# Kernel optimization log

Hardware: AMD Instinct MI355X
Metric: run time of the kernel (lower is better)

The kernel has to match this reference:

```python
import jax, jax.numpy as jnp
import numpy as np

B, S, D = 256, 512, 128
NQ, NC, NQD, NCD = 20000, 2000, 101, 101


def setup_inputs() -> dict:
    key = jax.random.key(0)
    ks = jax.random.split(key, 32)
    s = 0.05
    inp = {
        "question_seq": jax.random.randint(ks[0], (B, S), 0, NQ),
        "concept_seq": jax.random.randint(ks[1], (B, S), 0, NC),
        "question_diff_seq": jax.random.randint(ks[2], (B, S), 0, NQD),
        "concept_diff_seq": jax.random.randint(ks[3], (B, S), 0, NCD),
        "correct_seq": jax.random.randint(ks[4], (B, S), 0, 2),
        "E_q": jax.random.normal(ks[5], (NQ, D)) * s,
        "E_c": jax.random.normal(ks[6], (NC, D)) * s,
        "E_qd": jax.random.normal(ks[7], (NQD, D)) * s,
        "E_cd": jax.random.normal(ks[8], (NCD, D)) * s,
        "E_corr": jax.random.normal(ks[9], (2, D)) * s,
        "Wx": jax.random.normal(ks[10], (4 * D, D)) * s,
        "bx": jnp.zeros((D,)),
        "W_s1": jax.random.normal(ks[11], (D, D)) * s,
        "b_s1": jnp.zeros((D,)),
        "W_s2": jax.random.normal(ks[12], (D, D)) * s,
        "b_s2": jnp.zeros((D,)),
        "W_p1": jax.random.normal(ks[13], (2 * D, D)) * s,
        "b_p1": jnp.zeros((D,)),
        "W_p2": jax.random.normal(ks[14], (2 * D, D)) * s,
        "b_p2": jnp.zeros((D,)),
        "W_ki": jax.random.normal(ks[15], (4 * D, D)) * s,
        "b_ki": jnp.zeros((D,)),
        # xavier_uniform init of h_pre: bound = sqrt(6/(fan_in+fan_out))
        "h0": jax.random.uniform(ks[16], (B, D), minval=-1.0, maxval=1.0) * np.sqrt(6.0 / (B + D)),
    }
    return inp


def reference(question_seq, concept_seq, question_diff_seq, concept_diff_seq,
              correct_seq, E_q, E_c, E_qd, E_cd, E_corr,
              Wx, bx, W_s1, b_s1, W_s2, b_s2,
              W_p1, b_p1, W_p2, b_p2, W_ki, b_ki, h0):
    # embedding lookups: [B,S,D] each
    q = E_q[question_seq]
    c = E_c[concept_seq]
    qd = E_qd[question_diff_seq]
    cd = E_cd[concept_diff_seq]
    corr = E_corr[correct_seq]
    # generate_x_MLP applied to full sequence at once (loop-invariant)
    x = jnp.concatenate([q, c, qd, cd], axis=-1) @ Wx + bx  # [B,S,D]
    # time-major inputs for the recurrence over t = 0..S-2
    xs = jnp.swapaxes(x, 0, 1)          # [S,B,D]
    corr_t = jnp.swapaxes(corr, 0, 1)   # [S,B,D]
    qd_t = jnp.swapaxes(qd, 0, 1)
    cd_t = jnp.swapaxes(cd, 0, 1)

    def step(h, inp):
        x_t, x_next, co, qdt, cdt = inp
        d = x_t - h
        sdf = jax.nn.sigmoid(d @ W_s1 + b_s1) * jnp.tanh(d @ W_s2 + b_s2)  # dropout=eval
        pk_in = jnp.concatenate([sdf, co], axis=-1)
        pka = jax.nn.sigmoid(pk_in @ W_p1 + b_p1) * jnp.tanh(pk_in @ W_p2 + b_p2)
        ki_in = jnp.concatenate([h, co, qdt, cdt], axis=-1)
        g = jax.nn.sigmoid(ki_in @ W_ki + b_ki)
        h_new = g * h + (1.0 - g) * pka
        y_t = jax.nn.sigmoid(jnp.sum(x_next * h_new, axis=-1))  # [B]
        return h_new, y_t

    scan_in = (xs[:-1], xs[1:], corr_t[:-1], qd_t[:-1], cd_t[:-1])
    _, y_body = jax.lax.scan(step, h0, scan_in)  # y_body: [S-1,B]
    y = jnp.concatenate([y_body.T, jnp.zeros((question_seq.shape[0], 1), y_body.dtype)], axis=1)
    return y  # [B,S], last column zero as in original
```

## Files before the change

kernel.cpp:

```cpp
#include <hip/hip_runtime.h>

#define BB 256
#define SS 512
#define DD 128

__device__ __forceinline__ float sigf(float v) {
    return __builtin_amdgcn_rcpf(1.0f + __expf(-v));
}
__device__ __forceinline__ float tanhf_(float v) {
    return 1.0f - 2.0f * __builtin_amdgcn_rcpf(__expf(2.0f * v) + 1.0f);
}

__device__ __forceinline__ void lds_barrier() {
    asm volatile("s_waitcnt lgkmcnt(0)" ::: "memory");
    __builtin_amdgcn_s_barrier();
}

typedef _Float16 f16x2 __attribute__((ext_vector_type(2)));
typedef _Float16 f16x8 __attribute__((ext_vector_type(8)));
typedef float    f32x4 __attribute__((ext_vector_type(4)));

#define MFMA16(A, B, C) __builtin_amdgcn_mfma_f32_16x16x32_f16((A), (B), (C), 0, 0, 0)

#define N_EQ  (20000 * 128)
#define N_EC  (2000 * 128)
#define N_EQD (101 * 128)
#define N_ECD (101 * 128)
#define N_WXT (512 * 128)
#define N_WS  (128 * 128)
#define N_CVT (N_EQ + N_EC + N_EQD + N_ECD + N_WXT + 2 * N_WS)

__global__ __launch_bounds__(256) void dimkt_cvt(
    const float* __restrict__ E_q, const float* __restrict__ E_c,
    const float* __restrict__ E_qd, const float* __restrict__ E_cd,
    const float* __restrict__ Wx,
    const float* __restrict__ W_s1, const float* __restrict__ W_s2,
    _Float16* __restrict__ E_qh, _Float16* __restrict__ E_ch,
    _Float16* __restrict__ E_qdh, _Float16* __restrict__ E_cdh,
    _Float16* __restrict__ WxTh,
    _Float16* __restrict__ Ws1T, _Float16* __restrict__ Ws2T)
{
    int o = blockIdx.x * 256 + threadIdx.x;
    if (o >= N_CVT) return;
    if (o < N_EQ) { E_qh[o] = (_Float16)E_q[o]; return; }
    o -= N_EQ;
    if (o < N_EC) { E_ch[o] = (_Float16)E_c[o]; return; }
    o -= N_EC;
    if (o < N_EQD) { E_qdh[o] = (_Float16)E_qd[o]; return; }
    o -= N_EQD;
    if (o < N_ECD) { E_cdh[o] = (_Float16)E_cd[o]; return; }
    o -= N_ECD;
    if (o < N_WXT) {
        int n = o >> 9, k = o & 511;
        WxTh[o] = (_Float16)Wx[k * 128 + n];
        return;
    }
    o -= N_WXT;
    if (o < N_WS) {
        int n = o >> 7, k = o & 127;
        Ws1T[o] = (_Float16)W_s1[k * 128 + n];
        return;
    }
    o -= N_WS;
    {
        int n = o >> 7, k = o & 127;
        Ws2T[o] = (_Float16)W_s2[k * 128 + n];
    }
}

__global__ void dimkt_tables(const float* __restrict__ E_corr,
                             const float* __restrict__ E_qd,
                             const float* __restrict__ E_cd,
                             const float* __restrict__ W_ki,
                             const float* __restrict__ W_p1,
                             const float* __restrict__ W_p2,
                             const float* __restrict__ b_ki,
                             const float* __restrict__ b_p1,
                             const float* __restrict__ b_p2,
                             float* __restrict__ Ck, float* __restrict__ Cp1,
                             float* __restrict__ Cp2, float* __restrict__ Qk,
                             float* __restrict__ Cdk)
{
    __shared__ float e[128];
    const int r = blockIdx.x;
    const int j = threadIdx.x;
    const float *emb, *W, *bias;
    float* op;
    if (r < 2)        { emb = E_corr + r * 128;        W = W_ki + 128 * 128; bias = b_ki;    op = Ck  + r * 128; }
    else if (r < 4)   { emb = E_corr + (r - 2) * 128;  W = W_p1 + 128 * 128; bias = b_p1;    op = Cp1 + (r - 2) * 128; }
    else if (r < 6)   { emb = E_corr + (r - 4) * 128;  W = W_p2 + 128 * 128; bias = b_p2;    op = Cp2 + (r - 4) * 128; }
    else if (r < 107) { emb = E_qd   + (r - 6) * 128;  W = W_ki + 256 * 128; bias = nullptr; op = Qk  + (r - 6) * 128; }
    else              { emb = E_cd   + (r - 107) * 128; W = W_ki + 384 * 128; bias = nullptr; op = Cdk + (r - 107) * 128; }
    e[j] = emb[j];
    __syncthreads();
    float acc = bias ? bias[j] : 0.0f;
#pragma unroll 8
    for (int i = 0; i < 128; ++i) acc = fmaf(e[i], W[i * 128 + j], acc);
    op[j] = acc;
}

__global__ __launch_bounds__(256) void dimkt_strm(
    const int* __restrict__ corr_seq, const int* __restrict__ qd_seq,
    const int* __restrict__ cd_seq,
    const float* __restrict__ Ck, const float* __restrict__ Qk,
    const float* __restrict__ Cdk,
    const float* __restrict__ Cp1, const float* __restrict__ Cp2,
    _Float16* __restrict__ kgb, f16x2* __restrict__ Cp12h)
{
    const int row = blockIdx.x * 2 + (threadIdx.x >> 7);
    const int j   = threadIdx.x & 127;
    const int ic  = corr_seq[row];
    const int iq  = qd_seq[row];
    const int ie  = cd_seq[row];
    float v = Ck[ic * 128 + j] + Qk[iq * 128 + j] + Cdk[ie * 128 + j];
    kgb[(size_t)row * 128 + j] = (_Float16)v;
    if (blockIdx.x == 0) {
        int c = threadIdx.x >> 7, jj = threadIdx.x & 127;
        f16x2 t;
        t.x = (_Float16)Cp1[c * 128 + jj];
        t.y = (_Float16)Cp2[c * 128 + jj];
        Cp12h[c * 128 + jj] = t;
    }
}

__global__ __launch_bounds__(256, 2) void dimkt_xgemm(
    const int* __restrict__ q_seq, const int* __restrict__ c_seq,
    const int* __restrict__ qd_seq, const int* __restrict__ cd_seq,
    const _Float16* __restrict__ E_qh, const _Float16* __restrict__ E_ch,
    const _Float16* __restrict__ E_qdh, const _Float16* __restrict__ E_cdh,
    const _Float16* __restrict__ WxTh,
    const float* __restrict__ bx, _Float16* __restrict__ xh)
{
    const int tid = threadIdx.x;
    const int wv  = tid >> 6;
    const int l   = tid & 63;
    const int lm  = l & 15;
    const int kg8 = (l >> 4) * 8;
    const int m0  = blockIdx.x * 128;
    const int rbase = m0 + wv * 32;

    f32x4 acc0[8], acc1[8];
#pragma unroll
    for (int c = 0; c < 8; ++c) {
        acc0[c] = (f32x4){0.f, 0.f, 0.f, 0.f};
        acc1[c] = (f32x4){0.f, 0.f, 0.f, 0.f};
    }

#pragma unroll
    for (int s = 0; s < 4; ++s) {
        const _Float16* T  = (s == 0) ? E_qh : (s == 1) ? E_ch : (s == 2) ? E_qdh : E_cdh;
        const int*      sq = (s == 0) ? q_seq : (s == 1) ? c_seq : (s == 2) ? qd_seq : cd_seq;
        const int i0 = sq[rbase + lm];
        const int i1 = sq[rbase + 16 + lm];
        const _Float16* a0p = T + (size_t)i0 * 128 + kg8;
        const _Float16* a1p = T + (size_t)i1 * 128 + kg8;
#pragma unroll
        for (int kk = 0; kk < 4; ++kk) {
            const f16x8 a0 = *(const f16x8*)(a0p + kk * 32);
            const f16x8 a1 = *(const f16x8*)(a1p + kk * 32);
#pragma unroll
            for (int c = 0; c < 8; ++c) {
                const f16x8 bf = *(const f16x8*)&WxTh[(size_t)(c * 16 + lm) * 512
                                                      + s * 128 + kk * 32 + kg8];
                acc0[c] = MFMA16(a0, bf, acc0[c]);
                acc1[c] = MFMA16(a1, bf, acc1[c]);
            }
        }
    }

#pragma unroll
    for (int c = 0; c < 8; ++c) {
        const int col = c * 16 + lm;
        const float bxv = bx[col];
#pragma unroll
        for (int r = 0; r < 4; ++r) {
            const int row0 = rbase + (l >> 4) * 4 + r;
            xh[(size_t)row0 * 128 + col]        = (_Float16)(acc0[c][r] + bxv);
            xh[(size_t)(row0 + 16) * 128 + col] = (_Float16)(acc1[c][r] + bxv);
        }
    }
}

__global__ __launch_bounds__(256, 2) void dimkt_x12(
    const _Float16* __restrict__ xh,
    const _Float16* __restrict__ Ws1T, const _Float16* __restrict__ Ws2T,
    const float* __restrict__ b_s1, const float* __restrict__ b_s2,
    f16x2* __restrict__ X12)
{
    const int tid = threadIdx.x;
    const int wv  = tid >> 6;
    const int l   = tid & 63;
    const int lm  = l & 15;
    const int kg8 = (l >> 4) * 8;
    const int rbase = blockIdx.x * 128 + wv * 32;

    f32x4 acc0[16], acc1[16];
#pragma unroll
    for (int c = 0; c < 16; ++c) {
        acc0[c] = (f32x4){0.f, 0.f, 0.f, 0.f};
        acc1[c] = (f32x4){0.f, 0.f, 0.f, 0.f};
    }

    const _Float16* a0p = xh + (size_t)(rbase + lm) * 128 + kg8;
    const _Float16* a1p = xh + (size_t)(rbase + 16 + lm) * 128 + kg8;
#pragma unroll
    for (int kk = 0; kk < 4; ++kk) {
        const f16x8 a0 = *(const f16x8*)(a0p + kk * 32);
        const f16x8 a1 = *(const f16x8*)(a1p + kk * 32);
#pragma unroll
        for (int c = 0; c < 16; ++c) {
            const _Float16* BT = (c < 8) ? Ws1T : Ws2T;
            const f16x8 bf = *(const f16x8*)&BT[(size_t)((c & 7) * 16 + lm) * 128
                                                + kk * 32 + kg8];
            acc0[c] = MFMA16(a0, bf, acc0[c]);
            acc1[c] = MFMA16(a1, bf, acc1[c]);
        }
    }

#pragma unroll
    for (int c = 0; c < 8; ++c) {
        const int col = c * 16 + lm;
        const float bv1 = b_s1[col];
        const float bv2 = b_s2[col];
#pragma unroll
        for (int r = 0; r < 4; ++r) {
            const int row0 = rbase + (l >> 4) * 4 + r;
            f16x2 v0, v1;
            v0.x = (_Float16)(acc0[c][r] + bv1);
            v0.y = (_Float16)(acc0[c + 8][r] + bv2);
            v1.x = (_Float16)(acc1[c][r] + bv1);
            v1.y = (_Float16)(acc1[c + 8][r] + bv2);
            X12[(size_t)row0 * 128 + col]        = v0;
            X12[(size_t)(row0 + 16) * 128 + col] = v1;
        }
    }
}

__device__ __forceinline__ f16x8 load_wfrag(const float* __restrict__ W,
                                            int kbase, int j) {
    f16x8 r;
#pragma unroll
    for (int e = 0; e < 8; ++e) r[e] = (_Float16)W[(kbase + e) * DD + j];
    return r;
}
__device__ __forceinline__ f16x8 load_wfrag_neg(const float* __restrict__ W,
                                                int kbase, int j) {
    f16x8 r;
#pragma unroll
    for (int e = 0; e < 8; ++e) r[e] = (_Float16)(-W[(kbase + e) * DD + j]);
    return r;
}

__global__ __launch_bounds__(512, 2) void dimkt_scan(
    const f16x2* __restrict__ X12, const _Float16* __restrict__ kgb,
    const int* __restrict__ corr_seq, const f16x2* __restrict__ Cp12h,
    const float* __restrict__ W_s1, const float* __restrict__ W_s2,
    const float* __restrict__ W_p1, const float* __restrict__ W_p2,
    const float* __restrict__ W_ki,
    const float* __restrict__ h0, _Float16* __restrict__ hb,
    float* __restrict__ out)
{
    __shared__ __align__(16) _Float16 h_h[128];
    __shared__ __align__(16) _Float16 s_h[128];

    const int tid  = threadIdx.x;
    const int b    = blockIdx.x;
    const int wv   = tid >> 6;
    const int l    = tid & 63;
    const int kgrp = l >> 4;
    const int j    = wv * 16 + (l & 15);
    const int base = b * SS;

    const int kb = kgrp * 8;
    const f16x8 w1f0 = load_wfrag_neg(W_s1,  0 + kb, j);
    const f16x8 w1f1 = load_wfrag_neg(W_s1, 32 + kb, j);
    const f16x8 w1f2 = load_wfrag_neg(W_s1, 64 + kb, j);
    const f16x8 w1f3 = load_wfrag_neg(W_s1, 96 + kb, j);
    const f16x8 w2f0 = load_wfrag_neg(W_s2,  0 + kb, j);
    const f16x8 w2f1 = load_wfrag_neg(W_s2, 32 + kb, j);
    const f16x8 w2f2 = load_wfrag_neg(W_s2, 64 + kb, j);
    const f16x8 w2f3 = load_wfrag_neg(W_s2, 96 + kb, j);
    const f16x8 wkf0 = load_wfrag(W_ki,  0 + kb, j);
    const f16x8 wkf1 = load_wfrag(W_ki, 32 + kb, j);
    const f16x8 wkf2 = load_wfrag(W_ki, 64 + kb, j);
    const f16x8 wkf3 = load_wfrag(W_ki, 96 + kb, j);
    const f16x8 p1f0 = load_wfrag(W_p1,  0 + kb, j);
    const f16x8 p1f1 = load_wfrag(W_p1, 32 + kb, j);
    const f16x8 p1f2 = load_wfrag(W_p1, 64 + kb, j);
    const f16x8 p1f3 = load_wfrag(W_p1, 96 + kb, j);
    const f16x8 p2f0 = load_wfrag(W_p2,  0 + kb, j);
    const f16x8 p2f1 = load_wfrag(W_p2, 32 + kb, j);
    const f16x8 p2f2 = load_wfrag(W_p2, 64 + kb, j);
    const f16x8 p2f3 = load_wfrag(W_p2, 96 + kb, j);

    float h = h0[b * DD + j];
    if (kgrp == 0) h_h[j] = (_Float16)h;

    f16x2    X12v = X12[(size_t)base * DD + j];
    _Float16 kgt  = kgb[(size_t)base * DD + j];
    f16x2    cpv  = Cp12h[corr_seq[base] * DD + j];
    int icN = __builtin_amdgcn_readfirstlane(corr_seq[base + 1]);
    lds_barrier();

    const f32x4 z = {0.f, 0.f, 0.f, 0.f};

#pragma unroll 2
    for (int t = 0; t < 511; ++t) {
        const f16x8 hA0 = *(const f16x8*)&h_h[ 0 + kb];
        const f16x8 hA1 = *(const f16x8*)&h_h[32 + kb];
        const f16x8 hA2 = *(const f16x8*)&h_h[64 + kb];
        const f16x8 hA3 = *(const f16x8*)&h_h[96 + kb];

        f32x4 c1a = MFMA16(hA0, w1f0, z);
        f32x4 c2a = MFMA16(hA0, w2f0, z);
        f32x4 cka = MFMA16(hA0, wkf0, z);
        f32x4 c1b = MFMA16(hA2, w1f2, z);
        f32x4 c2b = MFMA16(hA2, w2f2, z);
        f32x4 ckb = MFMA16(hA2, wkf2, z);
        c1a = MFMA16(hA1, w1f1, c1a);
        c2a = MFMA16(hA1, w2f1, c2a);
        cka = MFMA16(hA1, wkf1, cka);
        c1b = MFMA16(hA3, w1f3, c1b);
        c2b = MFMA16(hA3, w2f3, c2b);
        ckb = MFMA16(hA3, wkf3, ckb);

        float a1 = (float)X12v.x + c1a[0] + c1b[0];
        float a2 = (float)X12v.y + c2a[0] + c2b[0];
        float sdf = sigf(a1) * tanhf_(a2);
        if (kgrp == 0) s_h[j] = (_Float16)sdf;
        float kg = cka[0] + ckb[0] + (float)kgt;
        lds_barrier();

        const f16x8 sA0 = *(const f16x8*)&s_h[ 0 + kb];
        const f16x8 sA1 = *(const f16x8*)&s_h[32 + kb];
        const f16x8 sA2 = *(const f16x8*)&s_h[64 + kb];
        const f16x8 sA3 = *(const f16x8*)&s_h[96 + kb];

        f32x4 q1a = MFMA16(sA0, p1f0, z);
        f32x4 q2a = MFMA16(sA0, p2f0, z);
        f32x4 q1b = MFMA16(sA2, p1f2, z);
        f32x4 q2b = MFMA16(sA2, p2f2, z);
        q1a = MFMA16(sA1, p1f1, q1a);
        q2a = MFMA16(sA1, p2f1, q2a);
        q1b = MFMA16(sA3, p1f3, q1b);
        q2b = MFMA16(sA3, p2f3, q2b);

        float g = sigf(kg);

        const size_t noff = (size_t)(base + t + 1) * DD + j;
        f16x2    nX12 = X12[noff];
        _Float16 nkgt = kgb[noff];
        f16x2    ncp  = Cp12h[icN * DD + j];
        const int n2 = base + ((t + 2 > 511) ? 511 : (t + 2));
        int icN2 = __builtin_amdgcn_readfirstlane(corr_seq[n2]);

        float pka = sigf(q1a[0] + q1b[0] + (float)cpv.x)
                  * tanhf_(q2a[0] + q2b[0] + (float)cpv.y);
        float hn  = fmaf(g, h - pka, pka);
        _Float16 hn16 = (_Float16)hn;
        if (kgrp == 0) {
            h_h[j] = hn16;
            hb[(size_t)(base + t) * DD + j] = hn16;
        }

        h = hn;
        X12v = nX12; kgt = nkgt; cpv = ncp; icN = icN2;
        lds_barrier();
    }

    if (tid == 0) out[base + 511] = 0.0f;
}

__global__ __launch_bounds__(256) void dimkt_y(
    const _Float16* __restrict__ xh, const _Float16* __restrict__ hb,
    float* __restrict__ out)
{
    const int o = blockIdx.x * 4 + (threadIdx.x >> 6);
    const int l = threadIdx.x & 63;
    const int b = o >> 9;
    const int t = o & 511;
    if (t == 511) return;
    f16x2 xv = *(const f16x2*)&xh[((size_t)(b * SS + t + 1)) * DD + 2 * l];
    f16x2 hv = *(const f16x2*)&hb[((size_t)(b * SS + t)) * DD + 2 * l];
    float s = (float)xv.x * (float)hv.x + (float)xv.y * (float)hv.y;
    s += __shfl_xor(s, 1);  s += __shfl_xor(s, 2);  s += __shfl_xor(s, 4);
    s += __shfl_xor(s, 8);  s += __shfl_xor(s, 16); s += __shfl_xor(s, 32);
    if (l == 0) out[b * SS + t] = sigf(s);
}

extern "C" void kernel_launch(void* const* d_in, const int* in_sizes, int n_in,
                              void* d_out, int out_size, void* d_ws, size_t ws_size,
                              hipStream_t stream) {
    const int*   q_seq    = (const int*)d_in[0];
    const int*   c_seq    = (const int*)d_in[1];
    const int*   qd_seq   = (const int*)d_in[2];
    const int*   cd_seq   = (const int*)d_in[3];
    const int*   corr_seq = (const int*)d_in[4];
    const float* E_q    = (const float*)d_in[5];
    const float* E_c    = (const float*)d_in[6];
    const float* E_qd   = (const float*)d_in[7];
    const float* E_cd   = (const float*)d_in[8];
    const float* E_corr = (const float*)d_in[9];
    const float* Wx     = (const float*)d_in[10];
    const float* bx     = (const float*)d_in[11];
    const float* W_s1   = (const float*)d_in[12];
    const float* b_s1   = (const float*)d_in[13];
    const float* W_s2   = (const float*)d_in[14];
    const float* b_s2   = (const float*)d_in[15];
    const float* W_p1   = (const float*)d_in[16];
    const float* b_p1   = (const float*)d_in[17];
    const float* W_p2   = (const float*)d_in[18];
    const float* b_p2   = (const float*)d_in[19];
    const float* W_ki   = (const float*)d_in[20];
    const float* b_ki   = (const float*)d_in[21];
    const float* h0     = (const float*)d_in[22];
    float* out = (float*)d_out;

    float* Ck   = (float*)d_ws;
    float* Cp1  = Ck  + 256;
    float* Cp2  = Cp1 + 256;
    float* Qk   = Cp2 + 256;
    float* Cdk  = Qk  + 101 * 128;
    _Float16* pool  = (_Float16*)((char*)d_ws + (size_t)131072);
    const size_t NBT = (size_t)BB * SS * DD;
    _Float16* xh    = pool;
    f16x2*    X12   = (f16x2*)(xh + NBT);
    _Float16* hbuf  = (_Float16*)(X12 + NBT);
    _Float16* kgb   = hbuf + NBT;
    f16x2*    Cp12h = (f16x2*)(kgb + NBT);
    _Float16* E_qh  = (_Float16*)(Cp12h + 256);
    _Float16* E_ch  = E_qh + N_EQ;
    _Float16* E_qdh = E_ch + N_EC;
    _Float16* E_cdh = E_qdh + N_EQD;
    _Float16* WxTh  = E_cdh + N_ECD;
    _Float16* Ws1T  = WxTh + N_WXT;
    _Float16* Ws2T  = Ws1T + N_WS;

    dimkt_cvt<<<(N_CVT + 255) / 256, 256, 0, stream>>>(
        E_q, E_c, E_qd, E_cd, Wx, W_s1, W_s2,
        E_qh, E_ch, E_qdh, E_cdh, WxTh, Ws1T, Ws2T);

    dimkt_tables<<<208, 128, 0, stream>>>(E_corr, E_qd, E_cd, W_ki, W_p1, W_p2,
                                          b_ki, b_p1, b_p2, Ck, Cp1, Cp2, Qk, Cdk);

    dimkt_strm<<<(BB * SS) / 2, 256, 0, stream>>>(corr_seq, qd_seq, cd_seq,
                                                  Ck, Qk, Cdk, Cp1, Cp2,
                                                  kgb, Cp12h);

    dimkt_xgemm<<<(BB * SS) / 128, 256, 0, stream>>>(q_seq, c_seq, qd_seq, cd_seq,
                                                     E_qh, E_ch, E_qdh, E_cdh,
                                                     WxTh, bx, xh);

    dimkt_x12<<<(BB * SS) / 128, 256, 0, stream>>>(xh, Ws1T, Ws2T, b_s1, b_s2,
                                                   X12);

    dimkt_scan<<<BB, 512, 0, stream>>>(X12, kgb, corr_seq, Cp12h,
                                       W_s1, W_s2, W_p1, W_p2, W_ki,
                                       h0, hbuf, out);

    dimkt_y<<<(BB * SS) / 4, 256, 0, stream>>>(xh, hbuf, out);
}
```

Before: 521.3 us.

## Fuse x GEMM with s1/s2 GEMM via LDS and simplify correctness table lookups

Merges the x-projection GEMM and the W_s1/W_s2 projection into a single kernel that stages the x tile in shared memory instead of re-reading it from global memory. The stream kernel becomes grid-stride with paired f16 stores. The scan now selects the two correctness bias rows from registers instead of gathering from a half-precision table each step. This removes one launch and one global pass over x, but the fused kernel uses more LDS, which may lower occupancy.

```diff
diff --git a/kernel.cpp b/kernel.cpp
--- a/kernel.cpp
+++ b/kernel.cpp
@@ -99,38 +99,39 @@
     op[j] = acc;
 }
 
-__global__ __launch_bounds__(256) void dimkt_strm(
+__global__ __launch_bounds__(256) void dimkt_strm2(
     const int* __restrict__ corr_seq, const int* __restrict__ qd_seq,
     const int* __restrict__ cd_seq,
     const float* __restrict__ Ck, const float* __restrict__ Qk,
     const float* __restrict__ Cdk,
-    const float* __restrict__ Cp1, const float* __restrict__ Cp2,
-    _Float16* __restrict__ kgb, f16x2* __restrict__ Cp12h)
-{
-    const int row = blockIdx.x * 2 + (threadIdx.x >> 7);
-    const int j   = threadIdx.x & 127;
-    const int ic  = corr_seq[row];
-    const int iq  = qd_seq[row];
-    const int ie  = cd_seq[row];
-    float v = Ck[ic * 128 + j] + Qk[iq * 128 + j] + Cdk[ie * 128 + j];
-    kgb[(size_t)row * 128 + j] = (_Float16)v;
-    if (blockIdx.x == 0) {
-        int c = threadIdx.x >> 7, jj = threadIdx.x & 127;
-        f16x2 t;
-        t.x = (_Float16)Cp1[c * 128 + jj];
-        t.y = (_Float16)Cp2[c * 128 + jj];
-        Cp12h[c * 128 + jj] = t;
-    }
-}
-
-__global__ __launch_bounds__(256, 2) void dimkt_xgemm(
+    _Float16* __restrict__ kgb)
+{
+    const int total = BB * SS * 64;
+    for (int v = blockIdx.x * 256 + threadIdx.x; v < total; v += 2048 * 256) {
+        const int row = v >> 6;
+        const int j2  = (v & 63) * 2;
+        const int ic  = corr_seq[row];
+        const int iq  = qd_seq[row];
+        const int ie  = cd_seq[row];
+        f16x2 o;
+        o.x = (_Float16)(Ck[ic * 128 + j2]     + Qk[iq * 128 + j2]     + Cdk[ie * 128 + j2]);
+        o.y = (_Float16)(Ck[ic * 128 + j2 + 1] + Qk[iq * 128 + j2 + 1] + Cdk[ie * 128 + j2 + 1]);
+        *(f16x2*)&kgb[(size_t)row * 128 + j2] = o;
+    }
+}
+
+__global__ __launch_bounds__(256, 2) void dimkt_feed(
     const int* __restrict__ q_seq, const int* __restrict__ c_seq,
     const int* __restrict__ qd_seq, const int* __restrict__ cd_seq,
     const _Float16* __restrict__ E_qh, const _Float16* __restrict__ E_ch,
     const _Float16* __restrict__ E_qdh, const _Float16* __restrict__ E_cdh,
-    const _Float16* __restrict__ WxTh,
-    const float* __restrict__ bx, _Float16* __restrict__ xh)
-{
+    const _Float16* __restrict__ WxTh, const float* __restrict__ bx,
+    const _Float16* __restrict__ Ws1T, const _Float16* __restrict__ Ws2T,
+    const float* __restrict__ b_s1, const float* __restrict__ b_s2,
+    _Float16* __restrict__ xh, f16x2* __restrict__ X12)
+{
+    __shared__ _Float16 xt[128][136];
+
     const int tid = threadIdx.x;
     const int wv  = tid >> 6;
     const int l   = tid & 63;
@@ -139,99 +140,88 @@
     const int m0  = blockIdx.x * 128;
     const int rbase = m0 + wv * 32;
 
-    f32x4 acc0[8], acc1[8];
-#pragma unroll
-    for (int c = 0; c < 8; ++c) {
-        acc0[c] = (f32x4){0.f, 0.f, 0.f, 0.f};
-        acc1[c] = (f32x4){0.f, 0.f, 0.f, 0.f};
-    }
-
-#pragma unroll
-    for (int s = 0; s < 4; ++s) {
-        const _Float16* T  = (s == 0) ? E_qh : (s == 1) ? E_ch : (s == 2) ? E_qdh : E_cdh;
-        const int*      sq = (s == 0) ? q_seq : (s == 1) ? c_seq : (s == 2) ? qd_seq : cd_seq;
-        const int i0 = sq[rbase + lm];
-        const int i1 = sq[rbase + 16 + lm];
-        const _Float16* a0p = T + (size_t)i0 * 128 + kg8;
-        const _Float16* a1p = T + (size_t)i1 * 128 + kg8;
+    {
+        f32x4 acc0[8], acc1[8];
+#pragma unroll
+        for (int c = 0; c < 8; ++c) {
+            acc0[c] = (f32x4){0.f, 0.f, 0.f, 0.f};
+            acc1[c] = (f32x4){0.f, 0.f, 0.f, 0.f};
+        }
+#pragma unroll
+        for (int s = 0; s < 4; ++s) {
+            const _Float16* T  = (s == 0) ? E_qh : (s == 1) ? E_ch : (s == 2) ? E_qdh : E_cdh;
+            const int*      sq = (s == 0) ? q_seq : (s == 1) ? c_seq : (s == 2) ? qd_seq : cd_seq;
+            const int i0 = sq[rbase + lm];
+            const int i1 = sq[rbase + 16 + lm];
+            const _Float16* a0p = T + (size_t)i0 * 128 + kg8;
+            const _Float16* a1p = T + (size_t)i1 * 128 + kg8;
+#pragma unroll
+            for (int kk = 0; kk < 4; ++kk) {
+                const f16x8 a0 = *(const f16x8*)(a0p + kk * 32);
+                const f16x8 a1 = *(const f16x8*)(a1p + kk * 32);
+#pragma unroll
+                for (int c = 0; c < 8; ++c) {
+                    const f16x8 bf = *(const f16x8*)&WxTh[(size_t)(c * 16 + lm) * 512
+                                                          + s * 128 + kk * 32 + kg8];
+                    acc0[c] = MFMA16(a0, bf, acc0[c]);
+                    acc1[c] = MFMA16(a1, bf, acc1[c]);
+                }
+            }
+        }
+#pragma unroll
+        for (int c = 0; c < 8; ++c) {
+            const int col = c * 16 + lm;
+            const float bxv = bx[col];
+#pragma unroll
+            for (int r = 0; r < 4; ++r) {
+                const int lr = wv * 32 + (l >> 4) * 4 + r;
+                _Float16 v0 = (_Float16)(acc0[c][r] + bxv);
+                _Float16 v1 = (_Float16)(acc1[c][r] + bxv);
+                xh[(size_t)(m0 + lr) * 128 + col]      = v0;
+                xh[(size_t)(m0 + lr + 16) * 128 + col] = v1;
+                xt[lr][col]      = v0;
+                xt[lr + 16][col] = v1;
+            }
+        }
+    }
+    __syncthreads();
+
+    {
+        f32x4 acc0[16], acc1[16];
+#pragma unroll
+        for (int c = 0; c < 16; ++c) {
+            acc0[c] = (f32x4){0.f, 0.f, 0.f, 0.f};
+            acc1[c] = (f32x4){0.f, 0.f, 0.f, 0.f};
+        }
 #pragma unroll
         for (int kk = 0; kk < 4; ++kk) {
-            const f16x8 a0 = *(const f16x8*)(a0p + kk * 32);
-            const f16x8 a1 = *(const f16x8*)(a1p + kk * 32);
-#pragma unroll
-            for (int c = 0; c < 8; ++c) {
-                const f16x8 bf = *(const f16x8*)&WxTh[(size_t)(c * 16 + lm) * 512
-                                                      + s * 128 + kk * 32 + kg8];
+            const f16x8 a0 = *(const f16x8*)&xt[wv * 32 + lm][kk * 32 + kg8];
+            const f16x8 a1 = *(const f16x8*)&xt[wv * 32 + 16 + lm][kk * 32 + kg8];
+#pragma unroll
+            for (int c = 0; c < 16; ++c) {
+                const _Float16* BT = (c < 8) ? Ws1T : Ws2T;
+                const f16x8 bf = *(const f16x8*)&BT[(size_t)((c & 7) * 16 + lm) * 128
+                                                    + kk * 32 + kg8];
                 acc0[c] = MFMA16(a0, bf, acc0[c]);
                 acc1[c] = MFMA16(a1, bf, acc1[c]);
             }
         }
-    }
-
-#pragma unroll
-    for (int c = 0; c < 8; ++c) {
-        const int col = c * 16 + lm;
-        const float bxv = bx[col];
-#pragma unroll
-        for (int r = 0; r < 4; ++r) {
-            const int row0 = rbase + (l >> 4) * 4 + r;
-            xh[(size_t)row0 * 128 + col]        = (_Float16)(acc0[c][r] + bxv);
-            xh[(size_t)(row0 + 16) * 128 + col] = (_Float16)(acc1[c][r] + bxv);
-        }
-    }
-}
-
-__global__ __launch_bounds__(256, 2) void dimkt_x12(
-    const _Float16* __restrict__ xh,
-    const _Float16* __restrict__ Ws1T, const _Float16* __restrict__ Ws2T,
-    const float* __restrict__ b_s1, const float* __restrict__ b_s2,
-    f16x2* __restrict__ X12)
-{
-    const int tid = threadIdx.x;
-    const int wv  = tid >> 6;
-    const int l   = tid & 63;
-    const int lm  = l & 15;
-    const int kg8 = (l >> 4) * 8;
-    const int rbase = blockIdx.x * 128 + wv * 32;
-
-    f32x4 acc0[16], acc1[16];
-#pragma unroll
-    for (int c = 0; c < 16; ++c) {
-        acc0[c] = (f32x4){0.f, 0.f, 0.f, 0.f};
-        acc1[c] = (f32x4){0.f, 0.f, 0.f, 0.f};
-    }
-
-    const _Float16* a0p = xh + (size_t)(rbase + lm) * 128 + kg8;
-    const _Float16* a1p = xh + (size_t)(rbase + 16 + lm) * 128 + kg8;
-#pragma unroll
-    for (int kk = 0; kk < 4; ++kk) {
-        const f16x8 a0 = *(const f16x8*)(a0p + kk * 32);
-        const f16x8 a1 = *(const f16x8*)(a1p + kk * 32);
-#pragma unroll
-        for (int c = 0; c < 16; ++c) {
-            const _Float16* BT = (c < 8) ? Ws1T : Ws2T;
-            const f16x8 bf = *(const f16x8*)&BT[(size_t)((c & 7) * 16 + lm) * 128
-                                                + kk * 32 + kg8];
-            acc0[c] = MFMA16(a0, bf, acc0[c]);
-            acc1[c] = MFMA16(a1, bf, acc1[c]);
-        }
-    }
-
-#pragma unroll
-    for (int c = 0; c < 8; ++c) {
-        const int col = c * 16 + lm;
-        const float bv1 = b_s1[col];
-        const float bv2 = b_s2[col];
-#pragma unroll
-        for (int r = 0; r < 4; ++r) {
-            const int row0 = rbase + (l >> 4) * 4 + r;
-            f16x2 v0, v1;
-            v0.x = (_Float16)(acc0[c][r] + bv1);
-            v0.y = (_Float16)(acc0[c + 8][r] + bv2);
-            v1.x = (_Float16)(acc1[c][r] + bv1);
-            v1.y = (_Float16)(acc1[c + 8][r] + bv2);
-            X12[(size_t)row0 * 128 + col]        = v0;
-            X12[(size_t)(row0 + 16) * 128 + col] = v1;
+#pragma unroll
+        for (int c = 0; c < 8; ++c) {
+            const int col = c * 16 + lm;
+            const float bv1 = b_s1[col];
+            const float bv2 = b_s2[col];
+#pragma unroll
+            for (int r = 0; r < 4; ++r) {
+                const int row0 = rbase + (l >> 4) * 4 + r;
+                f16x2 v0, v1;
+                v0.x = (_Float16)(acc0[c][r] + bv1);
+                v0.y = (_Float16)(acc0[c + 8][r] + bv2);
+                v1.x = (_Float16)(acc1[c][r] + bv1);
+                v1.y = (_Float16)(acc1[c + 8][r] + bv2);
+                X12[(size_t)row0 * 128 + col]        = v0;
+                X12[(size_t)(row0 + 16) * 128 + col] = v1;
+            }
         }
     }
 }
@@ -253,7 +243,8 @@
 
 __global__ __launch_bounds__(512, 2) void dimkt_scan(
     const f16x2* __restrict__ X12, const _Float16* __restrict__ kgb,
-    const int* __restrict__ corr_seq, const f16x2* __restrict__ Cp12h,
+    const int* __restrict__ corr_seq,
+    const float* __restrict__ Cp1f, const float* __restrict__ Cp2f,
     const float* __restrict__ W_s1, const float* __restrict__ W_s2,
     const float* __restrict__ W_p1, const float* __restrict__ W_p2,
     const float* __restrict__ W_ki,
@@ -293,12 +284,17 @@
     const f16x8 p2f2 = load_wfrag(W_p2, 64 + kb, j);
     const f16x8 p2f3 = load_wfrag(W_p2, 96 + kb, j);
 
+    const float cp1r0 = Cp1f[j],       cp2r0 = Cp2f[j];
+    const float cp1r1 = Cp1f[128 + j], cp2r1 = Cp2f[128 + j];
+
     float h = h0[b * DD + j];
     if (kgrp == 0) h_h[j] = (_Float16)h;
 
     f16x2    X12v = X12[(size_t)base * DD + j];
     _Float16 kgt  = kgb[(size_t)base * DD + j];
-    f16x2    cpv  = Cp12h[corr_seq[base] * DD + j];
+    int ic0 = __builtin_amdgcn_readfirstlane(corr_seq[base]);
+    float tcp1 = ic0 ? cp1r1 : cp1r0;
+    float tcp2 = ic0 ? cp2r1 : cp2r0;
     int icN = __builtin_amdgcn_readfirstlane(corr_seq[base + 1]);
     lds_barrier();
 
@@ -350,12 +346,13 @@
         const size_t noff = (size_t)(base + t + 1) * DD + j;
         f16x2    nX12 = X12[noff];
         _Float16 nkgt = kgb[noff];
-        f16x2    ncp  = Cp12h[icN * DD + j];
+        float ncp1 = icN ? cp1r1 : cp1r0;
+        float ncp2 = icN ? cp2r1 : cp2r0;
         const int n2 = base + ((t + 2 > 511) ? 511 : (t + 2));
         int icN2 = __builtin_amdgcn_readfirstlane(corr_seq[n2]);
 
-        float pka = sigf(q1a[0] + q1b[0] + (float)cpv.x)
-                  * tanhf_(q2a[0] + q2b[0] + (float)cpv.y);
+        float pka = sigf(q1a[0] + q1b[0] + tcp1)
+                  * tanhf_(q2a[0] + q2b[0] + tcp2);
         float hn  = fmaf(g, h - pka, pka);
         _Float16 hn16 = (_Float16)hn;
         if (kgrp == 0) {
@@ -364,7 +361,7 @@
         }
 
         h = hn;
-        X12v = nX12; kgt = nkgt; cpv = ncp; icN = icN2;
+        X12v = nX12; kgt = nkgt; tcp1 = ncp1; tcp2 = ncp2; icN = icN2;
         lds_barrier();
     }
 
@@ -427,8 +424,7 @@
     f16x2*    X12   = (f16x2*)(xh + NBT);
     _Float16* hbuf  = (_Float16*)(X12 + NBT);
     _Float16* kgb   = hbuf + NBT;
-    f16x2*    Cp12h = (f16x2*)(kgb + NBT);
-    _Float16* E_qh  = (_Float16*)(Cp12h + 256);
+    _Float16* E_qh  = kgb + NBT;
     _Float16* E_ch  = E_qh + N_EQ;
     _Float16* E_qdh = E_ch + N_EC;
     _Float16* E_cdh = E_qdh + N_EQD;
@@ -443,18 +439,15 @@
     dimkt_tables<<<208, 128, 0, stream>>>(E_corr, E_qd, E_cd, W_ki, W_p1, W_p2,
                                           b_ki, b_p1, b_p2, Ck, Cp1, Cp2, Qk, Cdk);
 
-    dimkt_strm<<<(BB * SS) / 2, 256, 0, stream>>>(corr_seq, qd_seq, cd_seq,
-                                                  Ck, Qk, Cdk, Cp1, Cp2,
-                                                  kgb, Cp12h);
-
-    dimkt_xgemm<<<(BB * SS) / 128, 256, 0, stream>>>(q_seq, c_seq, qd_seq, cd_seq,
-                                                     E_qh, E_ch, E_qdh, E_cdh,
-                                                     WxTh, bx, xh);
-
-    dimkt_x12<<<(BB * SS) / 128, 256, 0, stream>>>(xh, Ws1T, Ws2T, b_s1, b_s2,
-                                                   X12);
-
-    dimkt_scan<<<BB, 512, 0, stream>>>(X12, kgb, corr_seq, Cp12h,
+    dimkt_strm2<<<2048, 256, 0, stream>>>(corr_seq, qd_seq, cd_seq,
+                                          Ck, Qk, Cdk, kgb);
+
+    dimkt_feed<<<(BB * SS) / 128, 256, 0, stream>>>(
+        q_seq, c_seq, qd_seq, cd_seq,
+        E_qh, E_ch, E_qdh, E_cdh, WxTh, bx,
+        Ws1T, Ws2T, b_s1, b_s2, xh, X12);
+
+    dimkt_scan<<<BB, 512, 0, stream>>>(X12, kgb, corr_seq, Cp1, Cp2,
                                        W_s1, W_s2, W_p1, W_p2, W_ki,
                                        h0, hbuf, out);
 
```

Measured after the change: 489.1 us. 6.2% less time.
